# Optimization experiments

Measured on AMD Instinct MI355X. Metric: run time of the kernel, lower is better.

The kernel has to match this reference:

```python
import jax, jax.numpy as jnp
import numpy as np

N = 1024
D = 128          # node_dim
NUM_LAYERS = 3
H_CLS = 128      # edge classifier hidden


def setup_inputs() -> dict:
    key = jax.random.key(0)
    ks = jax.random.split(key, 20)
    s_in = 1.0 / np.sqrt(3.0)
    s_d = 1.0 / np.sqrt(D)
    s_2d = 1.0 / np.sqrt(2 * D)
    s_h = 1.0 / np.sqrt(H_CLS)
    inp = {
        "node_features": jax.random.uniform(ks[0], (N, 3), jnp.float32),
        "adj_matrix": jax.random.uniform(ks[1], (N, N), jnp.float32),
        "edge_weights": jax.random.normal(ks[2], (N, N, 1), jnp.float32),
        # node embedding Linear(3, D)
        "W_embed": jax.random.uniform(ks[3], (3, D), jnp.float32, -s_in, s_in),
        "b_embed": jax.random.uniform(ks[4], (D,), jnp.float32, -s_in, s_in),
        # stacked GCN layer params, [L, ...]
        "Wu": jax.random.uniform(ks[5], (NUM_LAYERS, D, D), jnp.float32, -s_d, s_d),
        "bu": jax.random.uniform(ks[6], (NUM_LAYERS, D), jnp.float32, -s_d, s_d),
        "Wv": jax.random.uniform(ks[7], (NUM_LAYERS, D, D), jnp.float32, -s_d, s_d),
        "bv": jax.random.uniform(ks[8], (NUM_LAYERS, D), jnp.float32, -s_d, s_d),
        "Wg": jax.random.uniform(ks[9], (NUM_LAYERS, 2 * D, D), jnp.float32, -s_2d, s_2d),
        "bg": jax.random.uniform(ks[10], (NUM_LAYERS, D), jnp.float32, -s_2d, s_2d),
        # edge classifier: Linear(2D, 128) -> ReLU -> Linear(128, 1)
        "Wc1": jax.random.uniform(ks[11], (2 * D, H_CLS), jnp.float32, -s_2d, s_2d),
        "bc1": jax.random.uniform(ks[12], (H_CLS,), jnp.float32, -s_2d, s_2d),
        "Wc2": jax.random.uniform(ks[13], (H_CLS, 1), jnp.float32, -s_h, s_h),
        "bc2": jax.random.uniform(ks[14], (1,), jnp.float32, -s_h, s_h),
    }
    return inp


def reference(node_features, adj_matrix, edge_weights,
              W_embed, b_embed, Wu, bu, Wv, bv, Wg, bg,
              Wc1, bc1, Wc2, bc2):
    h = node_features @ W_embed + b_embed                       # [N, D]
    for l in range(NUM_LAYERS):
        u = h @ Wu[l] + bu[l]                                   # [N, D]
        v = h @ Wv[l] + bv[l]                                   # [N, D]
        agg = adj_matrix @ v                                    # [N, D]
        # gate Linear(2D, D) on cat([u, agg]) == u @ Wg[:D] + agg @ Wg[D:]
        gate = jax.nn.sigmoid(u @ Wg[l, :D] + agg @ Wg[l, D:] + bg[l])
        h = jax.nn.relu(h + gate * agg)
    # edge classifier: cat([h_i, h_j]) @ Wc1 == (h @ Wc1[:D])[i] + (h @ Wc1[D:])[j]
    hi = h @ Wc1[:D]                                            # [N, H]
    hj = h @ Wc1[D:]                                            # [N, H]
    hidden = jax.nn.relu(hi[:, None, :] + hj[None, :, :] + bc1) # [N, N, H]
    logits = jnp.einsum('ijh,h->ij', hidden, Wc2[:, 0]) + bc2[0]  # [N, N]
    loss = jnp.mean(jnp.square(logits * adj_matrix - edge_weights[..., 0]))
    return logits, loss
```

## Files before the change

kernel.cpp:

```cpp
#include <hip/hip_runtime.h>

#define NN 1024
#define DD 128

typedef __attribute__((ext_vector_type(8))) __bf16 bf16x8;
typedef __attribute__((ext_vector_type(4))) float f32x4;

__device__ __forceinline__ float us2f(unsigned short b) { return __uint_as_float(((unsigned)b) << 16); }
__device__ __forceinline__ unsigned short f2bf(float f) {
    unsigned x = __float_as_uint(f);
    return (unsigned short)((x + 0x7fffu + ((x >> 16) & 1u)) >> 16);
}

__global__ __launch_bounds__(256) void k_prep_embuv(
    const float* __restrict__ adj, unsigned short* __restrict__ aH, unsigned short* __restrict__ aL,
    const float* __restrict__ nf, const float* __restrict__ We, const float* __restrict__ be,
    const float* __restrict__ Wu, const float* __restrict__ bu,
    const float* __restrict__ Wv, const float* __restrict__ bv,
    float* __restrict__ h, float* __restrict__ u,
    unsigned short* __restrict__ vTh, unsigned short* __restrict__ vTl,
    float* __restrict__ lossAcc, unsigned* __restrict__ counter)
{
    __shared__ float hS[4][DD];
    int b = blockIdx.x, tid = threadIdx.x;
    if (b < 1024) {
        int idx = (b * 256 + tid) * 4;
        float4 a = *(const float4*)(adj + idx);
        ushort4 hv, lv;
        hv.x = f2bf(a.x); lv.x = f2bf(a.x - us2f(hv.x));
        hv.y = f2bf(a.y); lv.y = f2bf(a.y - us2f(hv.y));
        hv.z = f2bf(a.z); lv.z = f2bf(a.z - us2f(hv.z));
        hv.w = f2bf(a.w); lv.w = f2bf(a.w - us2f(hv.w));
        *(ushort4*)(aH + idx) = hv;
        *(ushort4*)(aL + idx) = lv;
        if (b == 0 && tid == 0) { *lossAcc = 0.f; *counter = 0u; }
        return;
    }
    int m0 = (b - 1024) * 4;
    int d = tid & 127, half = tid >> 7;
    float hr[4];
#pragma unroll
    for (int r = 0; r < 4; ++r) {
        float a = be[d];
#pragma unroll
        for (int k = 0; k < 3; ++k) a = fmaf(nf[(m0 + r) * 3 + k], We[k * DD + d], a);
        hr[r] = a;
    }
    if (half == 0) {
#pragma unroll
        for (int r = 0; r < 4; ++r) { h[(m0 + r) * DD + d] = hr[r]; hS[r][d] = hr[r]; }
    }
    __syncthreads();
    const float* W = half ? Wv : Wu;
    float acc[4] = {0.f, 0.f, 0.f, 0.f};
#pragma unroll 4
    for (int k4 = 0; k4 < DD; k4 += 4) {
        f32x4 h0 = *(const f32x4*)&hS[0][k4];
        f32x4 h1 = *(const f32x4*)&hS[1][k4];
        f32x4 h2 = *(const f32x4*)&hS[2][k4];
        f32x4 h3 = *(const f32x4*)&hS[3][k4];
#pragma unroll
        for (int kk = 0; kk < 4; ++kk) {
            float w = W[(k4 + kk) * DD + d];
            acc[0] = fmaf(h0[kk], w, acc[0]);
            acc[1] = fmaf(h1[kk], w, acc[1]);
            acc[2] = fmaf(h2[kk], w, acc[2]);
            acc[3] = fmaf(h3[kk], w, acc[3]);
        }
    }
    if (half == 0) {
        float bb = bu[d];
#pragma unroll
        for (int r = 0; r < 4; ++r) u[(m0 + r) * DD + d] = acc[r] + bb;
    } else {
        float bb = bv[d];
        float v0 = acc[0] + bb, v1 = acc[1] + bb, v2 = acc[2] + bb, v3 = acc[3] + bb;
        ushort4 hv, lv;
        hv.x = f2bf(v0); lv.x = f2bf(v0 - us2f(hv.x));
        hv.y = f2bf(v1); lv.y = f2bf(v1 - us2f(hv.y));
        hv.z = f2bf(v2); lv.z = f2bf(v2 - us2f(hv.z));
        hv.w = f2bf(v3); lv.w = f2bf(v3 - us2f(hv.w));
        *(ushort4*)(vTh + d * NN + m0) = hv;
        *(ushort4*)(vTl + d * NN + m0) = lv;
    }
}

__global__ __launch_bounds__(256) void k_agg(
    const unsigned short* __restrict__ adjH, const unsigned short* __restrict__ adjL,
    const unsigned short* __restrict__ vTh, const unsigned short* __restrict__ vTl,
    float* __restrict__ P)
{
    int tid = threadIdx.x, lane = tid & 63, w = tid >> 6;
    int b = blockIdx.x;
    int nt = b >> 7;
    int mt = (b >> 1) & 63;
    int kc = ((b & 1) << 2) | w;
    int m = lane & 15, quad = lane >> 4;
    int k0 = kc * 128 + quad * 8;
    const unsigned short* ah = adjH + (size_t)(mt * 16 + m) * NN + k0;
    const unsigned short* al = adjL + (size_t)(mt * 16 + m) * NN + k0;
    const unsigned short* bh = vTh + (size_t)(nt * 16 + m) * NN + k0;
    const unsigned short* bl = vTl + (size_t)(nt * 16 + m) * NN + k0;
    f32x4 acc = {0.f, 0.f, 0.f, 0.f};
#pragma unroll
    for (int kt = 0; kt < 4; ++kt) {
        bf16x8 aH = *(const bf16x8*)(ah + kt * 32);
        bf16x8 aL = *(const bf16x8*)(al + kt * 32);
        bf16x8 bH = *(const bf16x8*)(bh + kt * 32);
        bf16x8 bL = *(const bf16x8*)(bl + kt * 32);
        acc = __builtin_amdgcn_mfma_f32_16x16x32_bf16(aH, bH, acc, 0, 0, 0);
        acc = __builtin_amdgcn_mfma_f32_16x16x32_bf16(aH, bL, acc, 0, 0, 0);
        acc = __builtin_amdgcn_mfma_f32_16x16x32_bf16(aL, bH, acc, 0, 0, 0);
    }
    float* Pk = P + (size_t)kc * (NN * DD);
    int row0 = mt * 16 + quad * 4;
    int col = nt * 16 + m;
#pragma unroll
    for (int r = 0; r < 4; ++r) Pk[(row0 + r) * DD + col] = acc[r];
}

__global__ __launch_bounds__(256) void k_gateuv(
    const float* __restrict__ P, float* __restrict__ u, float* __restrict__ h,
    const float* __restrict__ Wg, const float* __restrict__ bg,
    const float* __restrict__ Wun, const float* __restrict__ bun,
    const float* __restrict__ Wvn, const float* __restrict__ bvn,
    unsigned short* __restrict__ vTh, unsigned short* __restrict__ vTl)
{
    __shared__ float uS[4][DD], aS[4][DD], hS[4][DD];
    int tid = threadIdx.x;
    int m0 = blockIdx.x * 4;
    int d = tid & 127, half = tid >> 7;
#pragma unroll
    for (int e = tid; e < 512; e += 256) {
        int r = e >> 7, dd = e & 127;
        int idx = (m0 + r) * DD + dd;
        float s = 0.f;
#pragma unroll
        for (int c = 0; c < 8; ++c) s += P[(size_t)c * (NN * DD) + idx];
        aS[r][dd] = s;
        uS[r][dd] = u[idx];
    }
    __syncthreads();
    const float* WA = Wg;
    const float* WB = Wg + DD * DD;
    int r0 = half * 2;
    float acc[2] = {0.f, 0.f};
#pragma unroll 4
    for (int k4 = 0; k4 < DD; k4 += 4) {
        f32x4 u0 = *(const f32x4*)&uS[r0][k4];
        f32x4 u1 = *(const f32x4*)&uS[r0 + 1][k4];
        f32x4 a0 = *(const f32x4*)&aS[r0][k4];
        f32x4 a1 = *(const f32x4*)&aS[r0 + 1][k4];
#pragma unroll
        for (int kk = 0; kk < 4; ++kk) {
            float wa = WA[(k4 + kk) * DD + d];
            float wb = WB[(k4 + kk) * DD + d];
            acc[0] = fmaf(u0[kk], wa, fmaf(a0[kk], wb, acc[0]));
            acc[1] = fmaf(u1[kk], wa, fmaf(a1[kk], wb, acc[1]));
        }
    }
    float bgd = bg[d];
#pragma unroll
    for (int rr = 0; rr < 2; ++rr) {
        int r = r0 + rr;
        float g = 1.f / (1.f + __expf(-(acc[rr] + bgd)));
        float nh = fmaf(g, aS[r][d], h[(m0 + r) * DD + d]);
        nh = nh > 0.f ? nh : 0.f;
        h[(m0 + r) * DD + d] = nh;
        hS[r][d] = nh;
    }
    __syncthreads();
    const float* W = half ? Wvn : Wun;
    float av[4] = {0.f, 0.f, 0.f, 0.f};
#pragma unroll 4
    for (int k4 = 0; k4 < DD; k4 += 4) {
        f32x4 h0 = *(const f32x4*)&hS[0][k4];
        f32x4 h1 = *(const f32x4*)&hS[1][k4];
        f32x4 h2 = *(const f32x4*)&hS[2][k4];
        f32x4 h3 = *(const f32x4*)&hS[3][k4];
#pragma unroll
        for (int kk = 0; kk < 4; ++kk) {
            float w = W[(k4 + kk) * DD + d];
            av[0] = fmaf(h0[kk], w, av[0]);
            av[1] = fmaf(h1[kk], w, av[1]);
            av[2] = fmaf(h2[kk], w, av[2]);
            av[3] = fmaf(h3[kk], w, av[3]);
        }
    }
    if (half == 0) {
        float bb = bun[d];
#pragma unroll
        for (int r = 0; r < 4; ++r) u[(m0 + r) * DD + d] = av[r] + bb;
    } else {
        float bb = bvn[d];
        float v0 = av[0] + bb, v1 = av[1] + bb, v2 = av[2] + bb, v3 = av[3] + bb;
        ushort4 hv, lv;
        hv.x = f2bf(v0); lv.x = f2bf(v0 - us2f(hv.x));
        hv.y = f2bf(v1); lv.y = f2bf(v1 - us2f(hv.y));
        hv.z = f2bf(v2); lv.z = f2bf(v2 - us2f(hv.z));
        hv.w = f2bf(v3); lv.w = f2bf(v3 - us2f(hv.w));
        *(ushort4*)(vTh + d * NN + m0) = hv;
        *(ushort4*)(vTl + d * NN + m0) = lv;
    }
}

__global__ __launch_bounds__(256) void k_gatecls(
    const float* __restrict__ P, float* __restrict__ u, float* __restrict__ h,
    const float* __restrict__ Wg, const float* __restrict__ bg,
    const float* __restrict__ Wc1, const float* __restrict__ bc1, const float* __restrict__ Wc2,
    float* __restrict__ hi, float* __restrict__ hj,
    float* __restrict__ S1, float* __restrict__ S2)
{
    __shared__ float uS[4][DD], aS[4][DD], hS[4][DD];
    __shared__ float sred[2][4];
    int tid = threadIdx.x;
    int m0 = blockIdx.x * 4;
    int d = tid & 127, half = tid >> 7;
    if (tid < 8) sred[tid >> 2][tid & 3] = 0.f;
#pragma unroll
    for (int e = tid; e < 512; e += 256) {
        int r = e >> 7, dd = e & 127;
        int idx = (m0 + r) * DD + dd;
        float s = 0.f;
#pragma unroll
        for (int c = 0; c < 8; ++c) s += P[(size_t)c * (NN * DD) + idx];
        aS[r][dd] = s;
        uS[r][dd] = u[idx];
    }
    __syncthreads();
    const float* WA = Wg;
    const float* WB = Wg + DD * DD;
    int r0 = half * 2;
    float acc[2] = {0.f, 0.f};
#pragma unroll 4
    for (int k4 = 0; k4 < DD; k4 += 4) {
        f32x4 u0 = *(const f32x4*)&uS[r0][k4];
        f32x4 u1 = *(const f32x4*)&uS[r0 + 1][k4];
        f32x4 a0 = *(const f32x4*)&aS[r0][k4];
        f32x4 a1 = *(const f32x4*)&aS[r0 + 1][k4];
#pragma unroll
        for (int kk = 0; kk < 4; ++kk) {
            float wa = WA[(k4 + kk) * DD + d];
            float wb = WB[(k4 + kk) * DD + d];
            acc[0] = fmaf(u0[kk], wa, fmaf(a0[kk], wb, acc[0]));
            acc[1] = fmaf(u1[kk], wa, fmaf(a1[kk], wb, acc[1]));
        }
    }
    float bgd = bg[d];
#pragma unroll
    for (int rr = 0; rr < 2; ++rr) {
        int r = r0 + rr;
        float g = 1.f / (1.f + __expf(-(acc[rr] + bgd)));
        float nh = fmaf(g, aS[r][d], h[(m0 + r) * DD + d]);
        nh = nh > 0.f ? nh : 0.f;
        hS[r][d] = nh;
    }
    __syncthreads();
    const float* W = Wc1 + (half ? DD * DD : 0);
    float av[4] = {0.f, 0.f, 0.f, 0.f};
#pragma unroll 4
    for (int k4 = 0; k4 < DD; k4 += 4) {
        f32x4 h0 = *(const f32x4*)&hS[0][k4];
        f32x4 h1 = *(const f32x4*)&hS[1][k4];
        f32x4 h2 = *(const f32x4*)&hS[2][k4];
        f32x4 h3 = *(const f32x4*)&hS[3][k4];
#pragma unroll
        for (int kk = 0; kk < 4; ++kk) {
            float w = W[(k4 + kk) * DD + d];
            av[0] = fmaf(h0[kk], w, av[0]);
            av[1] = fmaf(h1[kk], w, av[1]);
            av[2] = fmaf(h2[kk], w, av[2]);
            av[3] = fmaf(h3[kk], w, av[3]);
        }
    }
    float wv = Wc2[d];
    float bcv = half ? 0.f : bc1[d];
    float* out = half ? hj : hi;
    int lane = tid & 63;
#pragma unroll
    for (int r = 0; r < 4; ++r) {
        float val = av[r] + bcv;
        out[(m0 + r) * DD + d] = val;
        float p = val * wv;
#pragma unroll
        for (int off = 32; off; off >>= 1) p += __shfl_down(p, off);
        if (lane == 0) atomicAdd(&sred[half][r], p);
    }
    __syncthreads();
    if (tid < 4) S1[m0 + tid] = sred[0][tid];
    else if (tid < 8) S2[m0 + tid - 4] = sred[1][tid - 4];
}

__global__ __launch_bounds__(256) void k_edge(
    const float* __restrict__ hi, const float* __restrict__ hj,
    const float* __restrict__ S1, const float* __restrict__ S2,
    const float* __restrict__ Wc2, const float* __restrict__ bc2,
    const float* __restrict__ adj, const float* __restrict__ ew,
    float* __restrict__ outL, float* __restrict__ lossAcc, unsigned* __restrict__ counter)
{
    __shared__ float hiT[128][68];
    __shared__ float hjT[128][68];
    __shared__ float wS[128];
    __shared__ float lred;
    int tid = threadIdx.x;
    int i0 = (blockIdx.x >> 4) * 64, j0 = (blockIdx.x & 15) * 64;
    if (tid == 0) lred = 0.f;
    if (tid < 128) wS[tid] = Wc2[tid];
    for (int e = tid; e < 64 * 128; e += 256) {
        int r = e >> 7, hh = e & 127;
        hiT[hh][r] = hi[(i0 + r) * DD + hh];
        hjT[hh][r] = hj[(j0 + r) * DD + hh];
    }
    __syncthreads();
    int tx = tid & 15, ty = tid >> 4;
    float acc[4][4] = {};
#pragma unroll 4
    for (int hh = 0; hh < 128; ++hh) {
        f32x4 a = *(const f32x4*)&hiT[hh][ty * 4];
        f32x4 b = *(const f32x4*)&hjT[hh][tx * 4];
        float w = wS[hh];
#pragma unroll
        for (int p = 0; p < 4; ++p)
#pragma unroll
            for (int q = 0; q < 4; ++q) {
                float x = a[p] + b[q];
                acc[p][q] = fmaf(fabsf(x), w, acc[p][q]);
            }
    }
    float bcv = bc2[0];
    float ls = 0.f;
#pragma unroll
    for (int p = 0; p < 4; ++p) {
        int i = i0 + ty * 4 + p;
        float s1 = S1[i];
        int jb = j0 + tx * 4;
        f32x4 s2 = *(const f32x4*)(S2 + jb);
        f32x4 lg;
#pragma unroll
        for (int q = 0; q < 4; ++q)
            lg[q] = fmaf(0.5f, acc[p][q] + s1 + s2[q], bcv);
        *(f32x4*)(outL + (size_t)i * NN + jb) = lg;
        f32x4 a4 = *(const f32x4*)(adj + (size_t)i * NN + jb);
        f32x4 e4 = *(const f32x4*)(ew + (size_t)i * NN + jb);
#pragma unroll
        for (int q = 0; q < 4; ++q) {
            float t = fmaf(lg[q], a4[q], -e4[q]);
            ls = fmaf(t, t, ls);
        }
    }
#pragma unroll
    for (int off = 32; off; off >>= 1) ls += __shfl_down(ls, off);
    if ((tid & 63) == 0) atomicAdd(&lred, ls);
    __syncthreads();
    if (tid == 0) {
        atomicAdd(lossAcc, lred);
        __threadfence();
        unsigned old = atomicAdd(counter, 1u);
        if (old == 255u) {
            __threadfence();
            outL[(size_t)NN * NN] = (*(volatile float*)lossAcc) * (1.f / (1024.f * 1024.f));
        }
    }
}

extern "C" void kernel_launch(void* const* d_in, const int* in_sizes, int n_in,
                              void* d_out, int out_size, void* d_ws, size_t ws_size,
                              hipStream_t stream)
{
    const float* nf  = (const float*)d_in[0];
    const float* adj = (const float*)d_in[1];
    const float* ew  = (const float*)d_in[2];
    const float* We  = (const float*)d_in[3];
    const float* be  = (const float*)d_in[4];
    const float* Wu  = (const float*)d_in[5];
    const float* bu  = (const float*)d_in[6];
    const float* Wv  = (const float*)d_in[7];
    const float* bv  = (const float*)d_in[8];
    const float* Wg  = (const float*)d_in[9];
    const float* bg  = (const float*)d_in[10];
    const float* Wc1 = (const float*)d_in[11];
    const float* bc1 = (const float*)d_in[12];
    const float* Wc2 = (const float*)d_in[13];
    const float* bc2 = (const float*)d_in[14];

    float* ws = (float*)d_ws;
    float* h   = ws;
    float* u   = ws + 131072;
    unsigned short* vTh = (unsigned short*)(ws + 262144);
    unsigned short* vTl = (unsigned short*)(ws + 327680);
    float* P   = ws + 393216;
    unsigned short* adjH = (unsigned short*)(ws + 1441792);
    unsigned short* adjL = (unsigned short*)(ws + 1966080);
    float* hi  = ws + 2490368;
    float* hj  = ws + 2621440;
    float* S1  = ws + 2752512;
    float* S2  = ws + 2753536;
    float* lossAcc = ws + 2754560;
    unsigned* counter = (unsigned*)(ws + 2754561);

    k_prep_embuv<<<1280, 256, 0, stream>>>(adj, adjH, adjL, nf, We, be,
                                           Wu, bu, Wv, bv, h, u, vTh, vTl, lossAcc, counter);
    for (int l = 0; l < 3; ++l) {
        k_agg<<<1024, 256, 0, stream>>>(adjH, adjL, vTh, vTl, P);
        if (l < 2)
            k_gateuv<<<256, 256, 0, stream>>>(P, u, h, Wg + l * 32768, bg + l * 128,
                                              Wu + (l + 1) * 16384, bu + (l + 1) * 128,
                                              Wv + (l + 1) * 16384, bv + (l + 1) * 128,
                                              vTh, vTl);
        else
            k_gatecls<<<256, 256, 0, stream>>>(P, u, h, Wg + 2 * 32768, bg + 2 * 128,
                                               Wc1, bc1, Wc2, hi, hj, S1, S2);
    }
    k_edge<<<256, 256, 0, stream>>>(hi, hj, S1, S2, Wc2, bc2, adj, ew,
                                    (float*)d_out, lossAcc, counter);
}
```

Measured before the change: 187.2 us.

## Fuse fp32 adjacency aggregation into per-layer gate kernel, drop bf16 split MFMA

```diff
diff --git a/kernel.cpp b/kernel.cpp
--- a/kernel.cpp
+++ b/kernel.cpp
@@ -3,52 +3,29 @@
 #define NN 1024
 #define DD 128
 
-typedef __attribute__((ext_vector_type(8))) __bf16 bf16x8;
 typedef __attribute__((ext_vector_type(4))) float f32x4;
 
-__device__ __forceinline__ float us2f(unsigned short b) { return __uint_as_float(((unsigned)b) << 16); }
-__device__ __forceinline__ unsigned short f2bf(float f) {
-    unsigned x = __float_as_uint(f);
-    return (unsigned short)((x + 0x7fffu + ((x >> 16) & 1u)) >> 16);
-}
-
-__global__ __launch_bounds__(256) void k_prep_embuv(
-    const float* __restrict__ adj, unsigned short* __restrict__ aH, unsigned short* __restrict__ aL,
+__global__ __launch_bounds__(256) void k_embuv(
     const float* __restrict__ nf, const float* __restrict__ We, const float* __restrict__ be,
     const float* __restrict__ Wu, const float* __restrict__ bu,
     const float* __restrict__ Wv, const float* __restrict__ bv,
-    float* __restrict__ h, float* __restrict__ u,
-    unsigned short* __restrict__ vTh, unsigned short* __restrict__ vTl,
-    float* __restrict__ lossAcc, unsigned* __restrict__ counter)
+    float* __restrict__ h, float* __restrict__ u, float* __restrict__ v,
+    unsigned* __restrict__ ctrl)
 {
     __shared__ float hS[4][DD];
     int b = blockIdx.x, tid = threadIdx.x;
-    if (b < 1024) {
-        int idx = (b * 256 + tid) * 4;
-        float4 a = *(const float4*)(adj + idx);
-        ushort4 hv, lv;
-        hv.x = f2bf(a.x); lv.x = f2bf(a.x - us2f(hv.x));
-        hv.y = f2bf(a.y); lv.y = f2bf(a.y - us2f(hv.y));
-        hv.z = f2bf(a.z); lv.z = f2bf(a.z - us2f(hv.z));
-        hv.w = f2bf(a.w); lv.w = f2bf(a.w - us2f(hv.w));
-        *(ushort4*)(aH + idx) = hv;
-        *(ushort4*)(aL + idx) = lv;
-        if (b == 0 && tid == 0) { *lossAcc = 0.f; *counter = 0u; }
-        return;
-    }
-    int m0 = (b - 1024) * 4;
+    if (b == 0 && tid < 4) ctrl[tid] = 0u;
+    int m0 = b * 4;
     int d = tid & 127, half = tid >> 7;
-    float hr[4];
-#pragma unroll
-    for (int r = 0; r < 4; ++r) {
-        float a = be[d];
-#pragma unroll
-        for (int k = 0; k < 3; ++k) a = fmaf(nf[(m0 + r) * 3 + k], We[k * DD + d], a);
-        hr[r] = a;
-    }
     if (half == 0) {
 #pragma unroll
-        for (int r = 0; r < 4; ++r) { h[(m0 + r) * DD + d] = hr[r]; hS[r][d] = hr[r]; }
+        for (int r = 0; r < 4; ++r) {
+            float a = be[d];
+#pragma unroll
+            for (int k = 0; k < 3; ++k) a = fmaf(nf[(m0 + r) * 3 + k], We[k * DD + d], a);
+            h[(m0 + r) * DD + d] = a;
+            hS[r][d] = a;
+        }
     }
     __syncthreads();
     const float* W = half ? Wv : Wu;
@@ -74,71 +51,49 @@
         for (int r = 0; r < 4; ++r) u[(m0 + r) * DD + d] = acc[r] + bb;
     } else {
         float bb = bv[d];
-        float v0 = acc[0] + bb, v1 = acc[1] + bb, v2 = acc[2] + bb, v3 = acc[3] + bb;
-        ushort4 hv, lv;
-        hv.x = f2bf(v0); lv.x = f2bf(v0 - us2f(hv.x));
-        hv.y = f2bf(v1); lv.y = f2bf(v1 - us2f(hv.y));
-        hv.z = f2bf(v2); lv.z = f2bf(v2 - us2f(hv.z));
-        hv.w = f2bf(v3); lv.w = f2bf(v3 - us2f(hv.w));
-        *(ushort4*)(vTh + d * NN + m0) = hv;
-        *(ushort4*)(vTl + d * NN + m0) = lv;
-    }
-}
-
-__global__ __launch_bounds__(256) void k_agg(
-    const unsigned short* __restrict__ adjH, const unsigned short* __restrict__ adjL,
-    const unsigned short* __restrict__ vTh, const unsigned short* __restrict__ vTl,
-    float* __restrict__ P)
-{
-    int tid = threadIdx.x, lane = tid & 63, w = tid >> 6;
-    int b = blockIdx.x;
-    int nt = b >> 7;
-    int mt = (b >> 1) & 63;
-    int kc = ((b & 1) << 2) | w;
-    int m = lane & 15, quad = lane >> 4;
-    int k0 = kc * 128 + quad * 8;
-    const unsigned short* ah = adjH + (size_t)(mt * 16 + m) * NN + k0;
-    const unsigned short* al = adjL + (size_t)(mt * 16 + m) * NN + k0;
-    const unsigned short* bh = vTh + (size_t)(nt * 16 + m) * NN + k0;
-    const unsigned short* bl = vTl + (size_t)(nt * 16 + m) * NN + k0;
-    f32x4 acc = {0.f, 0.f, 0.f, 0.f};
-#pragma unroll
-    for (int kt = 0; kt < 4; ++kt) {
-        bf16x8 aH = *(const bf16x8*)(ah + kt * 32);
-        bf16x8 aL = *(const bf16x8*)(al + kt * 32);
-        bf16x8 bH = *(const bf16x8*)(bh + kt * 32);
-        bf16x8 bL = *(const bf16x8*)(bl + kt * 32);
-        acc = __builtin_amdgcn_mfma_f32_16x16x32_bf16(aH, bH, acc, 0, 0, 0);
-        acc = __builtin_amdgcn_mfma_f32_16x16x32_bf16(aH, bL, acc, 0, 0, 0);
-        acc = __builtin_amdgcn_mfma_f32_16x16x32_bf16(aL, bH, acc, 0, 0, 0);
-    }
-    float* Pk = P + (size_t)kc * (NN * DD);
-    int row0 = mt * 16 + quad * 4;
-    int col = nt * 16 + m;
-#pragma unroll
-    for (int r = 0; r < 4; ++r) Pk[(row0 + r) * DD + col] = acc[r];
-}
-
-__global__ __launch_bounds__(256) void k_gateuv(
-    const float* __restrict__ P, float* __restrict__ u, float* __restrict__ h,
+#pragma unroll
+        for (int r = 0; r < 4; ++r) v[(m0 + r) * DD + d] = acc[r] + bb;
+    }
+}
+
+struct LSh {
+    float aggS[4][DD];
+    float uS[4][DD];
+    float hS[4][DD];
+    float sred[2][4];
+};
+
+__device__ __forceinline__ void agg_phase(
+    const float* __restrict__ adj, const float* __restrict__ vcur,
+    int m0, int tid, LSh* sh)
+{
+    int w = __builtin_amdgcn_readfirstlane(tid >> 6);
+    int c2 = (tid & 63) * 2;
+    const float* arow = adj + (size_t)(m0 + w) * NN;
+    float ax = 0.f, ay = 0.f;
+#pragma unroll 8
+    for (int k4 = 0; k4 < NN; k4 += 4) {
+        f32x4 a4 = *(const f32x4*)(arow + k4);
+#pragma unroll
+        for (int kk = 0; kk < 4; ++kk) {
+            float2 v2 = *(const float2*)(vcur + (k4 + kk) * DD + c2);
+            ax = fmaf(a4[kk], v2.x, ax);
+            ay = fmaf(a4[kk], v2.y, ay);
+        }
+    }
+    *(float2*)&sh->aggS[w][c2] = make_float2(ax, ay);
+    __syncthreads();
+}
+
+__device__ __forceinline__ void gate_phase(
+    const float* __restrict__ u, float* __restrict__ h,
     const float* __restrict__ Wg, const float* __restrict__ bg,
-    const float* __restrict__ Wun, const float* __restrict__ bun,
-    const float* __restrict__ Wvn, const float* __restrict__ bvn,
-    unsigned short* __restrict__ vTh, unsigned short* __restrict__ vTl)
-{
-    __shared__ float uS[4][DD], aS[4][DD], hS[4][DD];
-    int tid = threadIdx.x;
-    int m0 = blockIdx.x * 4;
-    int d = tid & 127, half = tid >> 7;
+    int m0, int tid, int d, int half, LSh* sh)
+{
 #pragma unroll
     for (int e = tid; e < 512; e += 256) {
         int r = e >> 7, dd = e & 127;
-        int idx = (m0 + r) * DD + dd;
-        float s = 0.f;
-#pragma unroll
-        for (int c = 0; c < 8; ++c) s += P[(size_t)c * (NN * DD) + idx];
-        aS[r][dd] = s;
-        uS[r][dd] = u[idx];
+        sh->uS[r][dd] = u[(m0 + r) * DD + dd];
     }
     __syncthreads();
     const float* WA = Wg;
@@ -147,10 +102,10 @@
     float acc[2] = {0.f, 0.f};
 #pragma unroll 4
     for (int k4 = 0; k4 < DD; k4 += 4) {
-        f32x4 u0 = *(const f32x4*)&uS[r0][k4];
-        f32x4 u1 = *(const f32x4*)&uS[r0 + 1][k4];
-        f32x4 a0 = *(const f32x4*)&aS[r0][k4];
-        f32x4 a1 = *(const f32x4*)&aS[r0 + 1][k4];
+        f32x4 u0 = *(const f32x4*)&sh->uS[r0][k4];
+        f32x4 u1 = *(const f32x4*)&sh->uS[r0 + 1][k4];
+        f32x4 a0 = *(const f32x4*)&sh->aggS[r0][k4];
+        f32x4 a1 = *(const f32x4*)&sh->aggS[r0 + 1][k4];
 #pragma unroll
         for (int kk = 0; kk < 4; ++kk) {
             float wa = WA[(k4 + kk) * DD + d];
@@ -164,20 +119,36 @@
     for (int rr = 0; rr < 2; ++rr) {
         int r = r0 + rr;
         float g = 1.f / (1.f + __expf(-(acc[rr] + bgd)));
-        float nh = fmaf(g, aS[r][d], h[(m0 + r) * DD + d]);
+        float nh = fmaf(g, sh->aggS[r][d], h[(m0 + r) * DD + d]);
         nh = nh > 0.f ? nh : 0.f;
+        sh->hS[r][d] = nh;
         h[(m0 + r) * DD + d] = nh;
-        hS[r][d] = nh;
-    }
-    __syncthreads();
+    }
+    __syncthreads();
+}
+
+__global__ __launch_bounds__(256) void k_layer(
+    const float* __restrict__ adj, const float* __restrict__ vcur,
+    float* __restrict__ u, float* __restrict__ h,
+    const float* __restrict__ Wg, const float* __restrict__ bg,
+    const float* __restrict__ Wun, const float* __restrict__ bun,
+    const float* __restrict__ Wvn, const float* __restrict__ bvn,
+    float* __restrict__ vnext)
+{
+    __shared__ LSh sh;
+    int b = blockIdx.x, tid = threadIdx.x;
+    int m0 = b * 4;
+    int d = tid & 127, half = tid >> 7;
+    agg_phase(adj, vcur, m0, tid, &sh);
+    gate_phase(u, h, Wg, bg, m0, tid, d, half, &sh);
     const float* W = half ? Wvn : Wun;
     float av[4] = {0.f, 0.f, 0.f, 0.f};
 #pragma unroll 4
     for (int k4 = 0; k4 < DD; k4 += 4) {
-        f32x4 h0 = *(const f32x4*)&hS[0][k4];
-        f32x4 h1 = *(const f32x4*)&hS[1][k4];
-        f32x4 h2 = *(const f32x4*)&hS[2][k4];
-        f32x4 h3 = *(const f32x4*)&hS[3][k4];
+        f32x4 h0 = *(const f32x4*)&sh.hS[0][k4];
+        f32x4 h1 = *(const f32x4*)&sh.hS[1][k4];
+        f32x4 h2 = *(const f32x4*)&sh.hS[2][k4];
+        f32x4 h3 = *(const f32x4*)&sh.hS[3][k4];
 #pragma unroll
         for (int kk = 0; kk < 4; ++kk) {
             float w = W[(k4 + kk) * DD + d];
@@ -187,83 +158,35 @@
             av[3] = fmaf(h3[kk], w, av[3]);
         }
     }
-    if (half == 0) {
-        float bb = bun[d];
-#pragma unroll
-        for (int r = 0; r < 4; ++r) u[(m0 + r) * DD + d] = av[r] + bb;
-    } else {
-        float bb = bvn[d];
-        float v0 = av[0] + bb, v1 = av[1] + bb, v2 = av[2] + bb, v3 = av[3] + bb;
-        ushort4 hv, lv;
-        hv.x = f2bf(v0); lv.x = f2bf(v0 - us2f(hv.x));
-        hv.y = f2bf(v1); lv.y = f2bf(v1 - us2f(hv.y));
-        hv.z = f2bf(v2); lv.z = f2bf(v2 - us2f(hv.z));
-        hv.w = f2bf(v3); lv.w = f2bf(v3 - us2f(hv.w));
-        *(ushort4*)(vTh + d * NN + m0) = hv;
-        *(ushort4*)(vTl + d * NN + m0) = lv;
-    }
-}
-
-__global__ __launch_bounds__(256) void k_gatecls(
-    const float* __restrict__ P, float* __restrict__ u, float* __restrict__ h,
+    float bb = half ? bvn[d] : bun[d];
+    float* out = half ? vnext : u;
+#pragma unroll
+    for (int r = 0; r < 4; ++r) out[(m0 + r) * DD + d] = av[r] + bb;
+}
+
+__global__ __launch_bounds__(256) void k_layercls(
+    const float* __restrict__ adj, const float* __restrict__ vcur,
+    float* __restrict__ u, float* __restrict__ h,
     const float* __restrict__ Wg, const float* __restrict__ bg,
     const float* __restrict__ Wc1, const float* __restrict__ bc1, const float* __restrict__ Wc2,
     float* __restrict__ hi, float* __restrict__ hj,
     float* __restrict__ S1, float* __restrict__ S2)
 {
-    __shared__ float uS[4][DD], aS[4][DD], hS[4][DD];
-    __shared__ float sred[2][4];
-    int tid = threadIdx.x;
-    int m0 = blockIdx.x * 4;
+    __shared__ LSh sh;
+    int b = blockIdx.x, tid = threadIdx.x;
+    int m0 = b * 4;
     int d = tid & 127, half = tid >> 7;
-    if (tid < 8) sred[tid >> 2][tid & 3] = 0.f;
-#pragma unroll
-    for (int e = tid; e < 512; e += 256) {
-        int r = e >> 7, dd = e & 127;
-        int idx = (m0 + r) * DD + dd;
-        float s = 0.f;
-#pragma unroll
-        for (int c = 0; c < 8; ++c) s += P[(size_t)c * (NN * DD) + idx];
-        aS[r][dd] = s;
-        uS[r][dd] = u[idx];
-    }
-    __syncthreads();
-    const float* WA = Wg;
-    const float* WB = Wg + DD * DD;
-    int r0 = half * 2;
-    float acc[2] = {0.f, 0.f};
-#pragma unroll 4
-    for (int k4 = 0; k4 < DD; k4 += 4) {
-        f32x4 u0 = *(const f32x4*)&uS[r0][k4];
-        f32x4 u1 = *(const f32x4*)&uS[r0 + 1][k4];
-        f32x4 a0 = *(const f32x4*)&aS[r0][k4];
-        f32x4 a1 = *(const f32x4*)&aS[r0 + 1][k4];
-#pragma unroll
-        for (int kk = 0; kk < 4; ++kk) {
-            float wa = WA[(k4 + kk) * DD + d];
-            float wb = WB[(k4 + kk) * DD + d];
-            acc[0] = fmaf(u0[kk], wa, fmaf(a0[kk], wb, acc[0]));
-            acc[1] = fmaf(u1[kk], wa, fmaf(a1[kk], wb, acc[1]));
-        }
-    }
-    float bgd = bg[d];
-#pragma unroll
-    for (int rr = 0; rr < 2; ++rr) {
-        int r = r0 + rr;
-        float g = 1.f / (1.f + __expf(-(acc[rr] + bgd)));
-        float nh = fmaf(g, aS[r][d], h[(m0 + r) * DD + d]);
-        nh = nh > 0.f ? nh : 0.f;
-        hS[r][d] = nh;
-    }
-    __syncthreads();
+    if (tid < 8) sh.sred[tid >> 2][tid & 3] = 0.f;
+    agg_phase(adj, vcur, m0, tid, &sh);
+    gate_phase(u, h, Wg, bg, m0, tid, d, half, &sh);
     const float* W = Wc1 + (half ? DD * DD : 0);
     float av[4] = {0.f, 0.f, 0.f, 0.f};
 #pragma unroll 4
     for (int k4 = 0; k4 < DD; k4 += 4) {
-        f32x4 h0 = *(const f32x4*)&hS[0][k4];
-        f32x4 h1 = *(const f32x4*)&hS[1][k4];
-        f32x4 h2 = *(const f32x4*)&hS[2][k4];
-        f32x4 h3 = *(const f32x4*)&hS[3][k4];
+        f32x4 h0 = *(const f32x4*)&sh.hS[0][k4];
+        f32x4 h1 = *(const f32x4*)&sh.hS[1][k4];
+        f32x4 h2 = *(const f32x4*)&sh.hS[2][k4];
+        f32x4 h3 = *(const f32x4*)&sh.hS[3][k4];
 #pragma unroll
         for (int kk = 0; kk < 4; ++kk) {
             float w = W[(k4 + kk) * DD + d];
@@ -284,11 +207,11 @@
         float p = val * wv;
 #pragma unroll
         for (int off = 32; off; off >>= 1) p += __shfl_down(p, off);
-        if (lane == 0) atomicAdd(&sred[half][r], p);
-    }
-    __syncthreads();
-    if (tid < 4) S1[m0 + tid] = sred[0][tid];
-    else if (tid < 8) S2[m0 + tid - 4] = sred[1][tid - 4];
+        if (lane == 0) atomicAdd(&sh.sred[half][r], p);
+    }
+    __syncthreads();
+    if (tid < 4) S1[m0 + tid] = sh.sred[0][tid];
+    else if (tid < 8) S2[m0 + tid - 4] = sh.sred[1][tid - 4];
 }
 
 __global__ __launch_bounds__(256) void k_edge(
@@ -296,7 +219,7 @@
     const float* __restrict__ S1, const float* __restrict__ S2,
     const float* __restrict__ Wc2, const float* __restrict__ bc2,
     const float* __restrict__ adj, const float* __restrict__ ew,
-    float* __restrict__ outL, float* __restrict__ lossAcc, unsigned* __restrict__ counter)
+    float* __restrict__ outL, unsigned* __restrict__ ctrl)
 {
     __shared__ float hiT[128][68];
     __shared__ float hjT[128][68];
@@ -317,13 +240,13 @@
 #pragma unroll 4
     for (int hh = 0; hh < 128; ++hh) {
         f32x4 a = *(const f32x4*)&hiT[hh][ty * 4];
-        f32x4 b = *(const f32x4*)&hjT[hh][tx * 4];
+        f32x4 bb = *(const f32x4*)&hjT[hh][tx * 4];
         float w = wS[hh];
 #pragma unroll
         for (int p = 0; p < 4; ++p)
 #pragma unroll
             for (int q = 0; q < 4; ++q) {
-                float x = a[p] + b[q];
+                float x = a[p] + bb[q];
                 acc[p][q] = fmaf(fabsf(x), w, acc[p][q]);
             }
     }
@@ -353,9 +276,10 @@
     if ((tid & 63) == 0) atomicAdd(&lred, ls);
     __syncthreads();
     if (tid == 0) {
+        float* lossAcc = (float*)(ctrl + 2);
         atomicAdd(lossAcc, lred);
         __threadfence();
-        unsigned old = atomicAdd(counter, 1u);
+        unsigned old = atomicAdd(ctrl + 1, 1u);
         if (old == 255u) {
             __threadfence();
             outL[(size_t)NN * NN] = (*(volatile float*)lossAcc) * (1.f / (1024.f * 1024.f));
@@ -386,31 +310,21 @@
     float* ws = (float*)d_ws;
     float* h   = ws;
     float* u   = ws + 131072;
-    unsigned short* vTh = (unsigned short*)(ws + 262144);
-    unsigned short* vTl = (unsigned short*)(ws + 327680);
-    float* P   = ws + 393216;
-    unsigned short* adjH = (unsigned short*)(ws + 1441792);
-    unsigned short* adjL = (unsigned short*)(ws + 1966080);
-    float* hi  = ws + 2490368;
-    float* hj  = ws + 2621440;
-    float* S1  = ws + 2752512;
-    float* S2  = ws + 2753536;
-    float* lossAcc = ws + 2754560;
-    unsigned* counter = (unsigned*)(ws + 2754561);
-
-    k_prep_embuv<<<1280, 256, 0, stream>>>(adj, adjH, adjL, nf, We, be,
-                                           Wu, bu, Wv, bv, h, u, vTh, vTl, lossAcc, counter);
-    for (int l = 0; l < 3; ++l) {
-        k_agg<<<1024, 256, 0, stream>>>(adjH, adjL, vTh, vTl, P);
-        if (l < 2)
-            k_gateuv<<<256, 256, 0, stream>>>(P, u, h, Wg + l * 32768, bg + l * 128,
-                                              Wu + (l + 1) * 16384, bu + (l + 1) * 128,
-                                              Wv + (l + 1) * 16384, bv + (l + 1) * 128,
-                                              vTh, vTl);
-        else
-            k_gatecls<<<256, 256, 0, stream>>>(P, u, h, Wg + 2 * 32768, bg + 2 * 128,
-                                               Wc1, bc1, Wc2, hi, hj, S1, S2);
-    }
+    float* v0  = ws + 262144;
+    float* v1  = ws + 393216;
+    float* hi  = ws + 524288;
+    float* hj  = ws + 655360;
+    float* S1  = ws + 786432;
+    float* S2  = ws + 787456;
+    unsigned* ctrl = (unsigned*)(ws + 788480);
+
+    k_embuv<<<256, 256, 0, stream>>>(nf, We, be, Wu, bu, Wv, bv, h, u, v0, ctrl);
+    k_layer<<<256, 256, 0, stream>>>(adj, v0, u, h, Wg, bg,
+                                     Wu + 16384, bu + 128, Wv + 16384, bv + 128, v1);
+    k_layer<<<256, 256, 0, stream>>>(adj, v1, u, h, Wg + 32768, bg + 128,
+                                     Wu + 32768, bu + 256, Wv + 32768, bv + 256, v0);
+    k_layercls<<<256, 256, 0, stream>>>(adj, v0, u, h, Wg + 65536, bg + 256,
+                                        Wc1, bc1, Wc2, hi, hj, S1, S2);
     k_edge<<<256, 256, 0, stream>>>(hi, hj, S1, S2, Wc2, bc2, adj, ew,
-                                    (float*)d_out, lossAcc, counter);
-}
+                                    (float*)d_out, ctrl);
+}
```

After: 240.3 us. +28.4%, slower.
